# Performance work log

Measured on AMD Instinct MI355X. Metric: run time of the kernel, lower is better.

The kernel has to match this reference:

```python
import jax, jax.numpy as jnp
import numpy as np

B, S, D = 16, 577, 768
H = 12
DH = D // H  # 64


def setup_inputs() -> dict:
    key = jax.random.key(0)
    ks = jax.random.split(key, 7)
    s = 0.02
    return {
        "hidden_states": jax.random.normal(ks[0], (B, S, D), dtype=jnp.float32),
        "wq": jax.random.normal(ks[1], (D, D), dtype=jnp.float32) * s,
        "bq": jnp.zeros((D,), dtype=jnp.float32),
        "wk": jax.random.normal(ks[2], (D, D), dtype=jnp.float32) * s,
        "bk": jnp.zeros((D,), dtype=jnp.float32),
        "wv": jax.random.normal(ks[3], (D, D), dtype=jnp.float32) * s,
        "bv": jnp.zeros((D,), dtype=jnp.float32),
    }


def reference(hidden_states, wq, bq, wk, bk, wv, bv):
    # Linear projections (torch nn.Linear: x @ W^T + b)
    q = hidden_states @ wq.T + bq  # [B,S,D]
    k = hidden_states @ wk.T + bk
    v = hidden_states @ wv.T + bv

    def split_heads(x):
        return x.reshape(B, S, H, DH).transpose(0, 2, 1, 3)  # [B,H,S,DH]

    q, k, v = split_heads(q), split_heads(k), split_heads(v)
    scale = 1.0 / jnp.sqrt(jnp.float32(DH))
    scores = jnp.einsum("bhqd,bhkd->bhqk", q, k) * scale  # [B,H,S,S]
    probs = jax.nn.softmax(scores, axis=-1)
    ctx = jnp.einsum("bhqk,bhkd->bhqd", probs, v)  # [B,H,S,DH]
    ctx = ctx.transpose(0, 2, 1, 3).reshape(B, S, D)
    return ctx, probs
```

## Files before the change

kernel.cpp:

```cpp
#include <hip/hip_runtime.h>
#include <hip/hip_bf16.h>
#include <cstdint>

#define B_  16
#define S_  577
#define D_  768
#define H_  12
#define SP  640
#define M_  (B_*S_)
#define MP  9344
#define N_  2304
#define SCS 664
#define QSCALE 0.18033688011112042f

typedef __attribute__((ext_vector_type(8))) short short8;
typedef __attribute__((ext_vector_type(4))) float f32x4;

static __device__ __forceinline__ unsigned short f2bf(float f) {
    uint32_t u = __builtin_bit_cast(uint32_t, f);
    uint32_t r = u + 0x7fffu + ((u >> 16) & 1u);
    return (unsigned short)(r >> 16);
}
static __device__ __forceinline__ float bf2f(unsigned short u) {
    uint32_t x = ((uint32_t)u) << 16;
    return __builtin_bit_cast(float, x);
}

typedef unsigned int u32;
typedef __attribute__((address_space(3))) u32 lds_u32;
typedef __attribute__((address_space(1))) const u32 gbl_u32;
static __device__ __forceinline__ void gll16(const void* g, void* l) {
    __builtin_amdgcn_global_load_lds((gbl_u32*)g, (lds_u32*)l, 16, 0, 0);
}


__global__ __launch_bounds__(256) void prep(
    const float* __restrict__ X,
    const float* __restrict__ Wq, const float* __restrict__ Wk, const float* __restrict__ Wv,
    unsigned short* __restrict__ Xb, unsigned short* __restrict__ Wb,
    unsigned short* __restrict__ Vf)
{
    const int NT1 = MP * 192;
    const int NT2 = N_ * 192;
    const int VPAD = 192 * 64 * 63;
    const int total = NT1 + NT2 + VPAD;
    const int stride = gridDim.x * 256;
    for (int i = blockIdx.x * 256 + threadIdx.x; i < total; i += stride) {
        if (i < NT1) {
            int row = i / 192, c4 = i - row * 192;
            uint2 out = make_uint2(0u, 0u);
            if (row < M_) {
                float4 v = *(const float4*)(X + (size_t)row * 768 + c4 * 4);
                unsigned short p[4] = { f2bf(v.x), f2bf(v.y), f2bf(v.z), f2bf(v.w) };
                out = *(uint2*)p;
            }
            *(uint2*)(Xb + (size_t)row * 768 + c4 * 4) = out;
        } else if (i < NT1 + NT2) {
            int j = i - NT1;
            int row = j / 192, c4 = j - row * 192;
            const float* src = (row < 768) ? (Wq + (size_t)row * 768)
                             : (row < 1536) ? (Wk + (size_t)(row - 768) * 768)
                                            : (Wv + (size_t)(row - 1536) * 768);
            float4 v = *(const float4*)(src + c4 * 4);
            unsigned short p[4] = { f2bf(v.x), f2bf(v.y), f2bf(v.z), f2bf(v.w) };
            *(uint2*)(Wb + (size_t)row * 768 + c4 * 4) = *(uint2*)p;
        } else {
            int j = i - NT1 - NT2;
            int bh = j / (64 * 63), rem = j - bh * (64 * 63);
            int d = rem / 63, key = 577 + (rem - d * 63);
            size_t off = (((size_t)bh * 20 + (key >> 5)) * 4 + (d >> 4)) * 512
                       + (d & 15) * 32 + ((key >> 3) & 3) * 8 + (key & 7);
            Vf[off] = 0;
        }
    }
}

__global__ __launch_bounds__(256) void qkv_gemm(
    const unsigned short* __restrict__ Xb, const unsigned short* __restrict__ Wb,
    const float* __restrict__ bq, const float* __restrict__ bk, const float* __restrict__ bv,
    unsigned short* __restrict__ Qf, unsigned short* __restrict__ Kf,
    unsigned short* __restrict__ Vf)
{
    __shared__ unsigned short Als[128 * 64];
    __shared__ unsigned short Bls[128 * 64];

    const int mt = blockIdx.x, nt = blockIdx.y;
    const bool qk = (nt < 12);
    const int tid = threadIdx.x, lane = tid & 63, wid = tid >> 6;
    const int wm = wid >> 1, wn = wid & 1;
    const int m0 = mt * 128, n0 = nt * 128;
    const int l15 = lane & 15, g = lane >> 4;
    const int prow = lane >> 3, pc8 = lane & 7;

    const unsigned short* Pa = qk ? Bls : Als;
    const unsigned short* Pb = qk ? Als : Bls;

    f32x4 acc[4][4] = {};

    for (int kk = 0; kk < 768; kk += 64) {
        __syncthreads();
        #pragma unroll
        for (int t = 0; t < 4; ++t) {
            int row  = wid * 32 + t * 8 + prow;
            int scol = ((pc8 ^ (row & 7)) * 8);
            gll16(Xb + (size_t)(m0 + row) * 768 + kk + scol, &Als[(wid * 32 + t * 8) * 64]);
            gll16(Wb + (size_t)(n0 + row) * 768 + kk + scol, &Bls[(wid * 32 + t * 8) * 64]);
        }
        __syncthreads();

        #pragma unroll
        for (int ks = 0; ks < 2; ++ks) {
            short8 fa[4], fb[4];
            #pragma unroll
            for (int i = 0; i < 4; ++i) {
                int row = wm * 64 + i * 16 + l15;
                fa[i] = *(const short8*)&Pa[row * 64 + (((ks * 4 + g) ^ (row & 7)) * 8)];
            }
            #pragma unroll
            for (int j = 0; j < 4; ++j) {
                int row = wn * 64 + j * 16 + l15;
                fb[j] = *(const short8*)&Pb[row * 64 + (((ks * 4 + g) ^ (row & 7)) * 8)];
            }
            #pragma unroll
            for (int i = 0; i < 4; ++i)
                #pragma unroll
                for (int j = 0; j < 4; ++j)
                    acc[i][j] = __builtin_amdgcn_mfma_f32_16x16x32_bf16(fa[i], fb[j], acc[i][j], 0, 0, 0);
        }
    }

    if (qk) {
        const float* bb = (nt < 6) ? bq : bk;
        unsigned short* Dst = (nt < 6) ? Qf : Kf;
        const float scale = (nt < 6) ? QSCALE : 1.0f;
        #pragma unroll
        for (int i = 0; i < 4; ++i) {
            int nrow0 = n0 - ((nt < 6) ? 0 : 768) + wm * 64 + i * 16 + g * 4;
            float4 b4 = *(const float4*)(bb + nrow0);
            int hh = nrow0 >> 6, d0 = nrow0 & 63;
            int dh5 = d0 >> 5;
            int dsub = ((d0 >> 3) & 3) * 8 + (d0 & 7);
            #pragma unroll
            for (int j = 0; j < 4; ++j) {
                int m = m0 + wn * 64 + j * 16 + l15;
                if (m >= M_) continue;
                int b = m / 577, s = m - b * 577;
                unsigned short p[4];
                p[0] = f2bf((acc[i][j][0] + b4.x) * scale);
                p[1] = f2bf((acc[i][j][1] + b4.y) * scale);
                p[2] = f2bf((acc[i][j][2] + b4.z) * scale);
                p[3] = f2bf((acc[i][j][3] + b4.w) * scale);
                size_t off;
                if (nt < 6)
                    off = (((size_t)(b * 40 + (s >> 4)) * 12 + hh) * 2 + dh5) * 512
                        + (s & 15) * 32 + dsub;
                else
                    off = ((((size_t)(b * 12 + hh)) * 10 + (s >> 6)) * 8 + ((s >> 4) & 3) * 2 + dh5) * 512
                        + (s & 15) * 32 + dsub;
                *(uint2*)(Dst + off) = *(uint2*)p;
            }
        }
    } else {
        #pragma unroll
        for (int j = 0; j < 4; ++j) {
            int n = n0 + wn * 64 + j * 16 + l15;
            int nn = n - 1536;
            float bias = bv[nn];
            int hh = nn >> 6, dwh = nn & 63;
            #pragma unroll
            for (int i = 0; i < 4; ++i) {
                #pragma unroll
                for (int r = 0; r < 4; ++r) {
                    int m = m0 + wm * 64 + i * 16 + g * 4 + r;
                    if (m >= M_) continue;
                    int b = m / 577, s = m - b * 577;
                    float val = acc[i][j][r] + bias;
                    size_t off = (((size_t)(b * 12 + hh) * 20 + (s >> 5)) * 4 + (dwh >> 4)) * 512
                               + (dwh & 15) * 32 + ((s >> 3) & 3) * 8 + (s & 7);
                    Vf[off] = f2bf(val);
                }
            }
        }
    }
}

__global__ __launch_bounds__(256) void attn(
    const unsigned short* __restrict__ Qf, const unsigned short* __restrict__ Kf,
    const unsigned short* __restrict__ Vf,
    float* __restrict__ ctx, float* __restrict__ probs)
{
    __shared__ unsigned short sc[16 * SCS];
    __shared__ float rowinv[16];

    const int wg  = blockIdx.x;
    const int idx = (wg & 7) * 888 + (wg >> 3);
    const int bh  = idx / 37;
    const int qt  = idx - bh * 37;
    const int h   = bh % 12, b = bh / 12;

    const int tid = threadIdx.x, lane = tid & 63, wid = tid >> 6;
    const int l15 = lane & 15, g = lane >> 4;
    const int q0 = qt * 16;
    const int lofs = l15 * 32 + g * 8;

    const unsigned short* qb = Qf + ((size_t)(b * 40 + qt) * 12 + h) * 1024 + lofs;
    short8 aq0 = *(const short8*)qb;
    short8 aq1 = *(const short8*)(qb + 512);

    const unsigned short* kb0 = Kf + (size_t)bh * 40960 + wid * 1024 + lofs;
    #pragma unroll
    for (int c = 0; c < 10; ++c) {
        const unsigned short* kb = kb0 + c * 4096;
        short8 bk0 = *(const short8*)kb;
        short8 bk1 = *(const short8*)(kb + 512);
        f32x4 s4 = {};
        s4 = __builtin_amdgcn_mfma_f32_16x16x32_bf16(aq0, bk0, s4, 0, 0, 0);
        s4 = __builtin_amdgcn_mfma_f32_16x16x32_bf16(aq1, bk1, s4, 0, 0, 0);
        int key = c * 64 + wid * 16 + l15;
        #pragma unroll
        for (int r = 0; r < 4; ++r)
            sc[(g * 4 + r) * SCS + key] = (key < S_) ? f2bf(s4[r]) : (unsigned short)0xFF80u;
    }
    __syncthreads();

    const int r = tid >> 4, c0 = tid & 15;
    unsigned short* row = &sc[r * SCS];
    float m = -1e30f;
    #pragma unroll
    for (int i = 0; i < 5; ++i) {
        short8 v = *(const short8*)&row[(c0 + 16 * i) * 8];
        #pragma unroll
        for (int jj = 0; jj < 8; ++jj) m = fmaxf(m, bf2f((unsigned short)v[jj]));
    }
    #pragma unroll
    for (int o = 8; o; o >>= 1) m = fmaxf(m, __shfl_xor(m, o));

    float ssum = 0.f;
    #pragma unroll
    for (int i = 0; i < 5; ++i) {
        short8 v = *(const short8*)&row[(c0 + 16 * i) * 8];
        short8 w;
        #pragma unroll
        for (int jj = 0; jj < 8; ++jj) {
            float e = exp2f(bf2f((unsigned short)v[jj]) - m);
            ssum += e;
            w[jj] = (short)f2bf(e);
        }
        *(short8*)&row[(c0 + 16 * i) * 8] = w;
    }
    #pragma unroll
    for (int o = 8; o; o >>= 1) ssum += __shfl_xor(ssum, o);
    float inv = 1.0f / ssum;
    if (c0 == 0) rowinv[r] = inv;
    __syncthreads();

    int q = q0 + r;
    if (q < S_) {
        float* prow = probs + ((size_t)bh * S_ + q) * S_;
        #pragma unroll
        for (int i = 0; i < 5; ++i) {
            int ch = c0 + 16 * i;
            short8 v = *(const short8*)&row[ch * 8];
            if (ch < 72) {
                f32x4 o0, o1;
                o0[0] = bf2f((unsigned short)v[0]) * inv; o0[1] = bf2f((unsigned short)v[1]) * inv;
                o0[2] = bf2f((unsigned short)v[2]) * inv; o0[3] = bf2f((unsigned short)v[3]) * inv;
                o1[0] = bf2f((unsigned short)v[4]) * inv; o1[1] = bf2f((unsigned short)v[5]) * inv;
                o1[2] = bf2f((unsigned short)v[6]) * inv; o1[3] = bf2f((unsigned short)v[7]) * inv;
                __builtin_nontemporal_store(o0, (f32x4*)&prow[ch * 8]);
                __builtin_nontemporal_store(o1, (f32x4*)&prow[ch * 8 + 4]);
            } else if (ch == 72) {
                __builtin_nontemporal_store(bf2f((unsigned short)v[0]) * inv, &prow[576]);
            }
        }
    }

    f32x4 oc = {};
    const unsigned short* vb0 = Vf + (size_t)bh * 40960 + wid * 512 + lofs;
    const unsigned short* pb  = &sc[l15 * SCS + g * 8];
    #pragma unroll
    for (int kk = 0; kk < 20; ++kk) {
        short8 ap = *(const short8*)(pb + kk * 32);
        short8 bv = *(const short8*)(vb0 + kk * 2048);
        oc = __builtin_amdgcn_mfma_f32_16x16x32_bf16(ap, bv, oc, 0, 0, 0);
    }
    #pragma unroll
    for (int rr = 0; rr < 4; ++rr) {
        int qr = g * 4 + rr;
        int qq = q0 + qr;
        if (qq < S_)
            __builtin_nontemporal_store(oc[rr] * rowinv[qr],
                &ctx[((size_t)b * S_ + qq) * D_ + h * 64 + wid * 16 + l15]);
    }
}

extern "C" void kernel_launch(void* const* d_in, const int* in_sizes, int n_in,
                              void* d_out, int out_size, void* d_ws, size_t ws_size,
                              hipStream_t stream) {
    const float* X  = (const float*)d_in[0];
    const float* Wq = (const float*)d_in[1];
    const float* bq = (const float*)d_in[2];
    const float* Wk = (const float*)d_in[3];
    const float* bk = (const float*)d_in[4];
    const float* Wv = (const float*)d_in[5];
    const float* bv = (const float*)d_in[6];

    float* ctx   = (float*)d_out;
    float* probs = ctx + (size_t)B_ * S_ * D_;

    unsigned short* Xb = (unsigned short*)probs;
    unsigned short* Wb = Xb + (size_t)MP * 768;

    unsigned short* Qf = (unsigned short*)d_ws;
    unsigned short* Kf = Qf + (size_t)7864320;
    unsigned short* Vf = Kf + (size_t)7864320;

    prep<<<dim3(1024), 256, 0, stream>>>(X, Wq, Wk, Wv, Xb, Wb, Vf);
    qkv_gemm<<<dim3(73, 18), 256, 0, stream>>>(Xb, Wb, bq, bk, bv, Qf, Kf, Vf);
    attn<<<dim3(7104), 256, 0, stream>>>(Qf, Kf, Vf, ctx, probs);
}
```

Measured before the change: 213.0 us.

## Swizzle QKV GEMM blocks per XCD and fuse probs store into PV loop

The QKV GEMM grid is flattened to 1D and remapped so each XCD handles a contiguous group of M tiles across all N tiles, with extra blocks exiting early. The aim is better L2 reuse of the X rows within each chiplet. In the attention kernel the softmax keeps its row values in registers instead of reading LDS twice. The probability write-out is moved into the P·V MFMA loop, reusing the A-operand fragments already loaded and spreading the stores across waves so they overlap with the matrix math. This adds branching inside the MFMA loop, and 1440 blocks are launched where 1314 do work.

```diff
diff --git a/kernel.cpp b/kernel.cpp
--- a/kernel.cpp
+++ b/kernel.cpp
@@ -84,7 +84,13 @@
     __shared__ unsigned short Als[128 * 64];
     __shared__ unsigned short Bls[128 * 64];
 
-    const int mt = blockIdx.x, nt = blockIdx.y;
+    const int bid = blockIdx.x;
+    const int xcd = bid & 7, sq = bid >> 3;
+    const int mtg = sq / 36, rem = sq - mtg * 36;
+    const int nt  = rem % 18;
+    const int mt  = xcd * 10 + mtg * 2 + rem / 18;
+    if (mt >= 73) return;
+
     const bool qk = (nt < 12);
     const int tid = threadIdx.x, lane = tid & 63, wid = tid >> 6;
     const int wm = wid >> 1, wn = wid & 1;
@@ -223,66 +229,65 @@
     }
     __syncthreads();
 
-    const int r = tid >> 4, c0 = tid & 15;
-    unsigned short* row = &sc[r * SCS];
-    float m = -1e30f;
-    #pragma unroll
-    for (int i = 0; i < 5; ++i) {
-        short8 v = *(const short8*)&row[(c0 + 16 * i) * 8];
-        #pragma unroll
-        for (int jj = 0; jj < 8; ++jj) m = fmaxf(m, bf2f((unsigned short)v[jj]));
-    }
-    #pragma unroll
-    for (int o = 8; o; o >>= 1) m = fmaxf(m, __shfl_xor(m, o));
-
-    float ssum = 0.f;
-    #pragma unroll
-    for (int i = 0; i < 5; ++i) {
-        short8 v = *(const short8*)&row[(c0 + 16 * i) * 8];
-        short8 w;
-        #pragma unroll
-        for (int jj = 0; jj < 8; ++jj) {
-            float e = exp2f(bf2f((unsigned short)v[jj]) - m);
-            ssum += e;
-            w[jj] = (short)f2bf(e);
-        }
-        *(short8*)&row[(c0 + 16 * i) * 8] = w;
-    }
-    #pragma unroll
-    for (int o = 8; o; o >>= 1) ssum += __shfl_xor(ssum, o);
-    float inv = 1.0f / ssum;
-    if (c0 == 0) rowinv[r] = inv;
+    {
+        const int r = tid >> 4, c0 = tid & 15;
+        unsigned short* row = &sc[r * SCS];
+        short8 v[5];
+        float m = -1e30f;
+        #pragma unroll
+        for (int i = 0; i < 5; ++i) {
+            v[i] = *(const short8*)&row[(c0 + 16 * i) * 8];
+            #pragma unroll
+            for (int jj = 0; jj < 8; ++jj) m = fmaxf(m, bf2f((unsigned short)v[i][jj]));
+        }
+        #pragma unroll
+        for (int o = 8; o; o >>= 1) m = fmaxf(m, __shfl_xor(m, o));
+
+        float ssum = 0.f;
+        #pragma unroll
+        for (int i = 0; i < 5; ++i) {
+            short8 w;
+            #pragma unroll
+            for (int jj = 0; jj < 8; ++jj) {
+                float e = exp2f(bf2f((unsigned short)v[i][jj]) - m);
+                ssum += e;
+                w[jj] = (short)f2bf(e);
+            }
+            *(short8*)&row[(c0 + 16 * i) * 8] = w;
+        }
+        #pragma unroll
+        for (int o = 8; o; o >>= 1) ssum += __shfl_xor(ssum, o);
+        if (c0 == 0) rowinv[r] = 1.0f / ssum;
+    }
     __syncthreads();
-
-    int q = q0 + r;
-    if (q < S_) {
-        float* prow = probs + ((size_t)bh * S_ + q) * S_;
-        #pragma unroll
-        for (int i = 0; i < 5; ++i) {
-            int ch = c0 + 16 * i;
-            short8 v = *(const short8*)&row[ch * 8];
-            if (ch < 72) {
-                f32x4 o0, o1;
-                o0[0] = bf2f((unsigned short)v[0]) * inv; o0[1] = bf2f((unsigned short)v[1]) * inv;
-                o0[2] = bf2f((unsigned short)v[2]) * inv; o0[3] = bf2f((unsigned short)v[3]) * inv;
-                o1[0] = bf2f((unsigned short)v[4]) * inv; o1[1] = bf2f((unsigned short)v[5]) * inv;
-                o1[2] = bf2f((unsigned short)v[6]) * inv; o1[3] = bf2f((unsigned short)v[7]) * inv;
-                __builtin_nontemporal_store(o0, (f32x4*)&prow[ch * 8]);
-                __builtin_nontemporal_store(o1, (f32x4*)&prow[ch * 8 + 4]);
-            } else if (ch == 72) {
-                __builtin_nontemporal_store(bf2f((unsigned short)v[0]) * inv, &prow[576]);
-            }
-        }
-    }
 
     f32x4 oc = {};
     const unsigned short* vb0 = Vf + (size_t)bh * 40960 + wid * 512 + lofs;
     const unsigned short* pb  = &sc[l15 * SCS + g * 8];
+    const bool qvalid = (q0 + l15) < S_;
+    const float pinv = rowinv[l15];
+    float* prow = probs + ((size_t)bh * S_ + q0 + l15) * S_;
     #pragma unroll
     for (int kk = 0; kk < 20; ++kk) {
         short8 ap = *(const short8*)(pb + kk * 32);
         short8 bv = *(const short8*)(vb0 + kk * 2048);
         oc = __builtin_amdgcn_mfma_f32_16x16x32_bf16(ap, bv, oc, 0, 0, 0);
+        if ((kk & 3) == wid) {
+            int kbase = kk * 32 + g * 8;
+            if (qvalid) {
+                if (kbase + 7 < S_) {
+                    f32x4 o0, o1;
+                    o0[0] = bf2f((unsigned short)ap[0]) * pinv; o0[1] = bf2f((unsigned short)ap[1]) * pinv;
+                    o0[2] = bf2f((unsigned short)ap[2]) * pinv; o0[3] = bf2f((unsigned short)ap[3]) * pinv;
+                    o1[0] = bf2f((unsigned short)ap[4]) * pinv; o1[1] = bf2f((unsigned short)ap[5]) * pinv;
+                    o1[2] = bf2f((unsigned short)ap[6]) * pinv; o1[3] = bf2f((unsigned short)ap[7]) * pinv;
+                    __builtin_nontemporal_store(o0, (f32x4*)&prow[kbase]);
+                    __builtin_nontemporal_store(o1, (f32x4*)&prow[kbase + 4]);
+                } else if (kbase < S_) {
+                    __builtin_nontemporal_store(bf2f((unsigned short)ap[0]) * pinv, &prow[576]);
+                }
+            }
+        }
     }
     #pragma unroll
     for (int rr = 0; rr < 4; ++rr) {
@@ -316,6 +321,6 @@
     unsigned short* Vf = Kf + (size_t)7864320;
 
     prep<<<dim3(1024), 256, 0, stream>>>(X, Wq, Wk, Wv, Xb, Wb, Vf);
-    qkv_gemm<<<dim3(73, 18), 256, 0, stream>>>(Xb, Wb, bq, bk, bv, Qf, Kf, Vf);
+    qkv_gemm<<<dim3(1440), 256, 0, stream>>>(Xb, Wb, bq, bk, bv, Qf, Kf, Vf);
     attn<<<dim3(7104), 256, 0, stream>>>(Qf, Kf, Vf, ctx, probs);
 }
```

Result: slower. 374.7 us (+75.9%).
